# Performance work log

Hardware: AMD Instinct MI355X
Metric: run time of the kernel (lower is better)

The kernel has to match this reference:

```python
import jax, jax.numpy as jnp
import numpy as np

THRESH = 0.3
LENS = 0.4
DECAY = 0.2


@jax.custom_vjp
def act_fun(x):
    return (x > THRESH).astype(x.dtype)

def _act_fwd(x):
    return act_fun(x), x

def _act_bwd(x, g):
    return (g * (jnp.abs(x - THRESH) < LENS).astype(g.dtype),)

act_fun.defvjp(_act_fwd, _act_bwd)


def _conv(x, w):
    # 3x3, stride 1, padding 1, NCHW/OIHW (no bias)
    return jax.lax.conv_general_dilated(
        x, w, (1, 1), ((1, 1), (1, 1)),
        dimension_numbers=("NCHW", "OIHW", "NCHW"))


def _pool2(x):
    # avg_pool2d(k=2) applied per trailing hh-channel: x is (B,C,H,W,4)
    B, C, H, W, K = x.shape
    return x.reshape(B, C, H // 2, 2, W // 2, 2, K).mean(axis=(3, 5))


def _mem_update(x, mem, spike):
    m = mem * DECAY * (1.0 - spike) + x
    return m, act_fun(m)


def _lif_step(drives3, inner, mem, spike):
    # drives3: 3 conv drives (B,C,H,W); inner drives channel 3
    ms, ss = [], []
    for k in range(3):
        m, s = _mem_update(drives3[k], mem[..., k], spike[..., k])
        ms.append(m); ss.append(s)
    m, s = _mem_update(inner, mem[..., 3], spike[..., 3])
    ms.append(m); ss.append(s)
    return jnp.stack(ms, axis=-1), jnp.stack(ss, axis=-1)


def setup_inputs() -> dict:
    key = jax.random.key(0)
    ks = jax.random.split(key, 11)
    B, T = 256, 3
    sc = 0.1
    return {
        "x": jax.random.normal(ks[0], (B, 1, 36, 36), jnp.float32),
        "w1": jax.random.normal(ks[1], (3, 10, 1, 3, 3), jnp.float32) * sc,
        "b1": jax.random.normal(ks[2], (3, 10), jnp.float32) * sc,
        "w2": jax.random.normal(ks[3], (3, 10, 10, 3, 3), jnp.float32) * sc,
        "b2": jax.random.normal(ks[4], (3, 10), jnp.float32) * sc,
        "lif_w": jax.random.normal(ks[5], (1, 3), jnp.float32) * sc,
        "lif_b": jax.random.normal(ks[6], (1,), jnp.float32) * sc,
        "fc_w": jax.random.normal(ks[7], (50, 3240), jnp.float32) * 0.02,
        "fc_b": jax.random.normal(ks[8], (50,), jnp.float32) * sc,
        "task_w": jax.random.normal(ks[9], (T, 10, 50), jnp.float32) * sc,
        "task_b": jax.random.normal(ks[10], (T, 10), jnp.float32) * sc,
        "time_window": 10,
    }


def reference(x, w1, b1, w2, b2, lif_w, lif_b, fc_w, fc_b, task_w, task_b, time_window):
    B = x.shape[0]
    c1_mem = jnp.zeros((B, 10, 36, 36, 4), x.dtype)
    c1_spk = jnp.zeros_like(c1_mem)
    c2_mem = jnp.zeros((B, 10, 18, 18, 4), x.dtype)
    c2_spk = jnp.zeros_like(c2_mem)
    h1 = jnp.zeros((B, 3240), x.dtype)

    # layer-1 drives depend only on the (constant) input: compute once
    drives1 = [_conv(x, w1[k]) + b1[k][:, None, None] for k in range(3)]

    def step(carry, _):
        c1_mem, c1_spk, c2_mem, c2_spk, h1 = carry
        # layer 1 (is_spike_input=False)
        inner1 = jnp.einsum("bchwk,ok->bchwo", c1_mem[..., 0:3], lif_w)[..., 0] + lif_b[0]
        c1_mem_n, c1_spk_n = _lif_step(drives1, inner1, c1_mem, c1_spk)
        p1 = _pool2(c1_spk_n)  # (B,10,18,18,4)
        # layer 2 (is_spike_input=True): sum of conv over 4 slices = conv(sum)+4*bias
        s = p1.sum(axis=-1)
        drives2 = [_conv(s, w2[k]) + 4.0 * b2[k][:, None, None] for k in range(3)]
        inner2 = jnp.einsum("bchwk,ok->bchwo", c2_mem[..., 0:3], lif_w)[..., 0] + lif_b[0]
        c2_mem_n, c2_spk_n = _lif_step(drives2, inner2, c2_mem, c2_spk)
        p2 = _pool2(c2_spk_n)  # (B,10,9,9,4)
        h1 = h1 + p2.reshape(B, -1)
        return (c1_mem_n, c1_spk_n, c2_mem_n, c2_spk_n, h1), None

    carry, _ = jax.lax.scan(step, (c1_mem, c1_spk, c2_mem, c2_spk, h1), None, length=time_window)
    h1 = carry[4]
    outs = (h1 / time_window) @ fc_w.T + fc_b  # (B,50)
    out = jnp.einsum("bf,tof->bto", outs, task_w) + task_b[None]  # (B,T,10)
    return out
```

## Files before the change

### kernel.cpp

```cpp
#include <hip/hip_runtime.h>

#define TH  0.3f
#define DEC 0.2f

#define OFF_X    0
#define OFF_W1   1596
#define OFF_B1   1876
#define OFF_W2   1908
#define OFF_B2   4708
#define OFF_LIF  4740
#define OFF_S    4744
#define OFF_C1X  9944
#define OFF_C2   12800
#define SMEM_N   26570

__device__ __forceinline__ float spikef(float v) { return v > TH ? 1.f : 0.f; }

__device__ __forceinline__ float ag_w(float v) {
    float a;
    asm("v_accvgpr_write_b32 %0, %1" : "=a"(a) : "v"(v));
    return a;
}
__device__ __forceinline__ float ag_r(float a) {
    float v;
    asm("v_accvgpr_read_b32 %0, %1" : "=v"(v) : "a"(a));
    return v;
}

#define AG16_DECL(P) \
    float P##0=ag_w(0.f), P##1=ag_w(0.f), P##2=ag_w(0.f), P##3=ag_w(0.f),   \
          P##4=ag_w(0.f), P##5=ag_w(0.f), P##6=ag_w(0.f), P##7=ag_w(0.f),   \
          P##8=ag_w(0.f), P##9=ag_w(0.f), P##10=ag_w(0.f), P##11=ag_w(0.f), \
          P##12=ag_w(0.f), P##13=ag_w(0.f), P##14=ag_w(0.f), P##15=ag_w(0.f)

#define LIF4(M, D0, D1, D2)                                            \
    {                                                                  \
        float inner_ = fmaf((M).x, lw0, fmaf((M).y, lw1, fmaf((M).z, lw2, lb))); \
        (M).x = ((M).x > TH ? 0.f : (M).x * DEC) + (D0);               \
        (M).y = ((M).y > TH ? 0.f : (M).y * DEC) + (D1);               \
        (M).z = ((M).z > TH ? 0.f : (M).z * DEC) + (D2);               \
        (M).w = ((M).w > TH ? 0.f : (M).w * DEC) + inner_;             \
    }

#define CONV27(WB, ACC)                                                      \
    do {                                                                     \
        float4 w4_;                                                          \
        _Pragma("unroll")                                                    \
        for (int j_ = 0; j_ < 27; ++j_) {                                    \
            if ((j_ & 3) == 0)                                               \
                w4_ = *reinterpret_cast<const float4*>(&sm[(WB) + j_]);      \
            const float wv_ = ((j_ & 3) == 0) ? w4_.x :                      \
                              ((j_ & 3) == 1) ? w4_.y :                      \
                              ((j_ & 3) == 2) ? w4_.z : w4_.w;               \
            const int k_ = j_ / 9, r_ = (j_ - k_ * 9) / 3,                   \
                      c_ = j_ - k_ * 9 - r_ * 3;                             \
            ACC(k_, r_, c_, wv_);                                            \
        }                                                                    \
    } while (0)

#define ACC_L1(K, R, C, W)                                   \
    d[0][K] = fmaf(xv[R][C],         (W), d[0][K]);          \
    d[1][K] = fmaf(xv[R][C + 1],     (W), d[1][K]);          \
    d[2][K] = fmaf(xv[R + 1][C],     (W), d[2][K]);          \
    d[3][K] = fmaf(xv[R + 1][C + 1], (W), d[3][K]);

#define ACC_L2(K, R, C, W)                                   \
    acc[0][K] = fmaf(sv[R][C],         (W), acc[0][K]);      \
    acc[1][K] = fmaf(sv[R][C + 1],     (W), acc[1][K]);      \
    acc[2][K] = fmaf(sv[R + 1][C],     (W), acc[2][K]);      \
    acc[3][K] = fmaf(sv[R + 1][C + 1], (W), acc[3][K]);

__device__ __forceinline__ void conv1(const float* __restrict__ sm, int cell,
                                      float (&d)[4][3])
{
    int oc  = cell / 324;
    int rem = cell - oc * 324;
    int hh  = rem / 18;
    int ww  = rem - hh * 18;
    int y0 = 2 * hh, x0 = 2 * ww;

    float xv[4][4];
#pragma unroll
    for (int r = 0; r < 4; ++r) {
        float2 a = *reinterpret_cast<const float2*>(&sm[OFF_X + (y0 + r) * 42 + x0]);
        float2 b = *reinterpret_cast<const float2*>(&sm[OFF_X + (y0 + r) * 42 + x0 + 2]);
        xv[r][0] = a.x; xv[r][1] = a.y; xv[r][2] = b.x; xv[r][3] = b.y;
    }
    {
        float b0  = sm[OFF_B1 + oc];
        float b1v = sm[OFF_B1 + 10 + oc];
        float b2v = sm[OFF_B1 + 20 + oc];
#pragma unroll
        for (int p = 0; p < 4; ++p) { d[p][0] = b0; d[p][1] = b1v; d[p][2] = b2v; }
    }
    CONV27(OFF_W1 + oc * 28, ACC_L1);
}

__device__ __forceinline__ void conv2(const float* __restrict__ sm, int cell,
                                      float (&acc)[4][3])
{
    int oc  = cell / 81;
    int rem = cell - oc * 81;
    int hh  = rem / 9;
    int ww  = rem - hh * 9;
    int y0 = 2 * hh, x0 = 2 * ww;

    {
        float b20 = 4.f * sm[OFF_B2 + oc];
        float b21 = 4.f * sm[OFF_B2 + 10 + oc];
        float b22 = 4.f * sm[OFF_B2 + 20 + oc];
#pragma unroll
        for (int p = 0; p < 4; ++p) { acc[p][0] = b20; acc[p][1] = b21; acc[p][2] = b22; }
    }

    const int sb = OFF_S + y0 * 26 + x0;
    const int wb = OFF_W2 + (oc * 10) * 28;

    for (int ic = 0; ic < 10; ++ic) {
        float sv[4][4];
#pragma unroll
        for (int r = 0; r < 4; ++r) {
            float2 a = *reinterpret_cast<const float2*>(&sm[sb + ic * 520 + r * 26]);
            float2 b = *reinterpret_cast<const float2*>(&sm[sb + ic * 520 + r * 26 + 2]);
            sv[r][0] = a.x; sv[r][1] = a.y; sv[r][2] = b.x; sv[r][3] = b.y;
        }
        CONV27(wb + ic * 28, ACC_L2);
    }
}

#define L1_AG_CELL(P, CELL)                                                   \
    {                                                                         \
        const int cell_ = (CELL);                                             \
        float d[4][3];                                                        \
        conv1(sm, cell_, d);                                                  \
        float ssum = 0.f; float4 m;                                           \
        m = make_float4(ag_r(P##0), ag_r(P##1), ag_r(P##2), ag_r(P##3));      \
        LIF4(m, d[0][0], d[0][1], d[0][2]);                                   \
        ssum += spikef(m.x) + spikef(m.y) + spikef(m.z) + spikef(m.w);        \
        P##0=ag_w(m.x); P##1=ag_w(m.y); P##2=ag_w(m.z); P##3=ag_w(m.w);       \
        m = make_float4(ag_r(P##4), ag_r(P##5), ag_r(P##6), ag_r(P##7));      \
        LIF4(m, d[1][0], d[1][1], d[1][2]);                                   \
        ssum += spikef(m.x) + spikef(m.y) + spikef(m.z) + spikef(m.w);        \
        P##4=ag_w(m.x); P##5=ag_w(m.y); P##6=ag_w(m.z); P##7=ag_w(m.w);       \
        m = make_float4(ag_r(P##8), ag_r(P##9), ag_r(P##10), ag_r(P##11));    \
        LIF4(m, d[2][0], d[2][1], d[2][2]);                                   \
        ssum += spikef(m.x) + spikef(m.y) + spikef(m.z) + spikef(m.w);        \
        P##8=ag_w(m.x); P##9=ag_w(m.y); P##10=ag_w(m.z); P##11=ag_w(m.w);     \
        m = make_float4(ag_r(P##12), ag_r(P##13), ag_r(P##14), ag_r(P##15));  \
        LIF4(m, d[3][0], d[3][1], d[3][2]);                                   \
        ssum += spikef(m.x) + spikef(m.y) + spikef(m.z) + spikef(m.w);        \
        P##12=ag_w(m.x); P##13=ag_w(m.y); P##14=ag_w(m.z); P##15=ag_w(m.w);   \
        int oc_ = cell_ / 324, rem_ = cell_ - oc_ * 324;                      \
        int hh_ = rem_ / 18, ww_ = rem_ - hh_ * 18;                           \
        sm[OFF_S + oc_ * 520 + (hh_ + 1) * 26 + (ww_ + 1)] = ssum * 0.25f;    \
    }

__attribute__((amdgpu_waves_per_eu(4, 4)))
__global__ __launch_bounds__(1024)
void scnn_kernel(const float* __restrict__ x,
                 const float* __restrict__ w1, const float* __restrict__ b1,
                 const float* __restrict__ w2, const float* __restrict__ b2,
                 const float* __restrict__ lif_w, const float* __restrict__ lif_b,
                 const float* __restrict__ fc_w, const float* __restrict__ fc_b,
                 const float* __restrict__ task_w, const float* __restrict__ task_b,
                 const int* __restrict__ tw_ptr,
                 float* __restrict__ out)
{
    __shared__ float sm[SMEM_N];
    const int tid = threadIdx.x;
    const int b   = blockIdx.x;
    const int T   = tw_ptr[0];

    for (int i = tid; i < SMEM_N; i += 1024) sm[i] = 0.f;
    __syncthreads();

    for (int i = tid; i < 1296; i += 1024) {
        int h = i / 36, w = i - h * 36;
        sm[OFF_X + (h + 1) * 42 + (w + 1)] = x[b * 1296 + i];
    }
    if (tid < 270) {
        int k = tid / 90, r = tid - k * 90;
        int oc = r / 9, j = r - oc * 9;
        sm[OFF_W1 + oc * 28 + k * 9 + j] = w1[tid];
    }
    if (tid < 30)  sm[OFF_B1 + tid] = b1[tid];
    for (int i = tid; i < 2700; i += 1024) {
        int k = i / 900, r1 = i - k * 900;
        int oc = r1 / 90, r2 = r1 - oc * 90;
        int ic = r2 / 9,  j  = r2 - ic * 9;
        sm[OFF_W2 + (oc * 10 + ic) * 28 + k * 9 + j] = w2[i];
    }
    if (tid < 30)  sm[OFF_B2 + tid] = b2[tid];
    if (tid < 3)   sm[OFF_LIF + tid] = lif_w[tid];
    if (tid == 0)  sm[OFF_LIF + 3] = lif_b[0];
    __syncthreads();

    const float lw0 = sm[OFF_LIF + 0], lw1 = sm[OFF_LIF + 1],
                lw2 = sm[OFF_LIF + 2], lb  = sm[OFF_LIF + 3];

    AG16_DECL(aA);
    AG16_DECL(aB);
    AG16_DECL(aC);
    float hA0=0.f,hA1=0.f,hA2=0.f,hA3=0.f;

    for (int t = 0; t < T; ++t) {
        L1_AG_CELL(aA, tid);
        __builtin_amdgcn_sched_barrier(0);
        L1_AG_CELL(aB, tid + 1024);
        __builtin_amdgcn_sched_barrier(0);
        L1_AG_CELL(aC, tid + 2048);
        __builtin_amdgcn_sched_barrier(0);
        if (tid < 3240 - 3072) {
            const int cell = tid + 3072;
            float d[4][3];
            conv1(sm, cell, d);
            float* cp = &sm[OFF_C1X + tid * 17];
            float ssum = 0.f;
#pragma unroll
            for (int p = 0; p < 4; ++p) {
                float4 m = make_float4(cp[4*p], cp[4*p+1], cp[4*p+2], cp[4*p+3]);
                LIF4(m, d[p][0], d[p][1], d[p][2]);
                ssum += spikef(m.x) + spikef(m.y) + spikef(m.z) + spikef(m.w);
                cp[4*p] = m.x; cp[4*p+1] = m.y; cp[4*p+2] = m.z; cp[4*p+3] = m.w;
            }
            int oc_ = cell / 324, rem_ = cell - oc_ * 324;
            int hh_ = rem_ / 18, ww_ = rem_ - hh_ * 18;
            sm[OFF_S + oc_ * 520 + (hh_ + 1) * 26 + (ww_ + 1)] = ssum * 0.25f;
        }
        __syncthreads();

        if (tid < 810) {
            float acc[4][3];
            conv2(sm, tid, acc);
            float* cp = &sm[OFF_C2 + tid * 17];
#pragma unroll
            for (int p = 0; p < 4; ++p) {
                float4 m = make_float4(cp[4*p], cp[4*p+1], cp[4*p+2], cp[4*p+3]);
                LIF4(m, acc[p][0], acc[p][1], acc[p][2]);
                hA0 += spikef(m.x) * 0.25f; hA1 += spikef(m.y) * 0.25f;
                hA2 += spikef(m.z) * 0.25f; hA3 += spikef(m.w) * 0.25f;
                cp[4*p] = m.x; cp[4*p+1] = m.y; cp[4*p+2] = m.z; cp[4*p+3] = m.w;
            }
        }
        __syncthreads();
    }

    if (tid < 810)
        *reinterpret_cast<float4*>(&sm[OFF_S + tid * 4]) = make_float4(hA0, hA1, hA2, hA3);
    __syncthreads();

    float invT = 1.f / (float)T;
    int f = tid >> 4, g = tid & 15;
    if (f < 50) {
        const float* wrow = fc_w + f * 3240;
        float p0 = 0.f, p1 = 0.f;
        for (int j = g; j + 16 < 3240; j += 32) {
            p0 = fmaf(sm[OFF_S + j], wrow[j], p0);
            p1 = fmaf(sm[OFF_S + j + 16], wrow[j + 16], p1);
        }
        { int j = 3232 + g; if (j < 3240) p0 = fmaf(sm[OFF_S + j], wrow[j], p0); }
        float p = p0 + p1;
        p += __shfl_xor(p, 1);
        p += __shfl_xor(p, 2);
        p += __shfl_xor(p, 4);
        p += __shfl_xor(p, 8);
        if (g == 0) sm[OFF_X + f] = p * invT + fc_b[f];
    }
    __syncthreads();

    if (tid < 30) {
        float acc = task_b[tid];
        const float* twp = task_w + tid * 50;
        for (int j = 0; j < 50; ++j) acc = fmaf(sm[OFF_X + j], twp[j], acc);
        out[b * 30 + tid] = acc;
    }
}

extern "C" void kernel_launch(void* const* d_in, const int* in_sizes, int n_in,
                              void* d_out, int out_size, void* d_ws, size_t ws_size,
                              hipStream_t stream) {
    const float* x      = (const float*)d_in[0];
    const float* w1     = (const float*)d_in[1];
    const float* b1     = (const float*)d_in[2];
    const float* w2     = (const float*)d_in[3];
    const float* b2     = (const float*)d_in[4];
    const float* lif_w  = (const float*)d_in[5];
    const float* lif_b  = (const float*)d_in[6];
    const float* fc_w   = (const float*)d_in[7];
    const float* fc_b   = (const float*)d_in[8];
    const float* task_w = (const float*)d_in[9];
    const float* task_b = (const float*)d_in[10];
    const int*   tw     = (const int*)d_in[11];

    int B = in_sizes[0] / 1296;

    scnn_kernel<<<B, 1024, 0, stream>>>(x, w1, b1, w2, b2, lif_w, lif_b,
                                        fc_w, fc_b, task_w, task_b, tw,
                                        (float*)d_out);
}
```

Measured before the change: 204.8 us.

## Double-buffer layer-1 spike map to remove one barrier per time step

Adds a second pooled-spike buffer in shared memory and software-pipelines the time loop. Layer-2 conv for step t reads one buffer while layer-1 for step t+1 writes the other, so one __syncthreads per iteration is dropped. Threads 810 and up no longer idle at a barrier during the layer-2 phase, and layer-1 work can overlap with it. The cost is about 20KB more LDS, which could limit blocks per CU, and a peeled first layer-1 pass.

```diff
diff --git a/kernel.cpp b/kernel.cpp
--- a/kernel.cpp
+++ b/kernel.cpp
@@ -9,10 +9,11 @@
 #define OFF_W2   1908
 #define OFF_B2   4708
 #define OFF_LIF  4740
-#define OFF_S    4744
-#define OFF_C1X  9944
-#define OFF_C2   12800
-#define SMEM_N   26570
+#define OFF_SA   4744
+#define OFF_SB   9944
+#define OFF_C1X  15144
+#define OFF_C2   18000
+#define SMEM_N   31770
 
 __device__ __forceinline__ float spikef(float v) { return v > TH ? 1.f : 0.f; }
 
@@ -96,7 +97,7 @@
     CONV27(OFF_W1 + oc * 28, ACC_L1);
 }
 
-__device__ __forceinline__ void conv2(const float* __restrict__ sm, int cell,
+__device__ __forceinline__ void conv2(const float* __restrict__ sm, int sbase, int cell,
                                       float (&acc)[4][3])
 {
     int oc  = cell / 81;
@@ -113,7 +114,7 @@
         for (int p = 0; p < 4; ++p) { acc[p][0] = b20; acc[p][1] = b21; acc[p][2] = b22; }
     }
 
-    const int sb = OFF_S + y0 * 26 + x0;
+    const int sb = sbase + y0 * 26 + x0;
     const int wb = OFF_W2 + (oc * 10) * 28;
 
     for (int ic = 0; ic < 10; ++ic) {
@@ -128,7 +129,7 @@
     }
 }
 
-#define L1_AG_CELL(P, CELL)                                                   \
+#define L1_AG_CELL(P, CELL, SB_)                                              \
     {                                                                         \
         const int cell_ = (CELL);                                             \
         float d[4][3];                                                        \
@@ -152,8 +153,28 @@
         P##12=ag_w(m.x); P##13=ag_w(m.y); P##14=ag_w(m.z); P##15=ag_w(m.w);   \
         int oc_ = cell_ / 324, rem_ = cell_ - oc_ * 324;                      \
         int hh_ = rem_ / 18, ww_ = rem_ - hh_ * 18;                           \
-        sm[OFF_S + oc_ * 520 + (hh_ + 1) * 26 + (ww_ + 1)] = ssum * 0.25f;    \
-    }
+        sm[(SB_) + oc_ * 520 + (hh_ + 1) * 26 + (ww_ + 1)] = ssum * 0.25f;    \
+    }
+
+__device__ __forceinline__ void l1_overflow(float* __restrict__ sm, int tid, int sbase,
+                                            float lw0, float lw1, float lw2, float lb)
+{
+    const int cell = tid + 3072;
+    float d[4][3];
+    conv1(sm, cell, d);
+    float* cp = &sm[OFF_C1X + tid * 17];
+    float ssum = 0.f;
+#pragma unroll
+    for (int p = 0; p < 4; ++p) {
+        float4 m = make_float4(cp[4*p], cp[4*p+1], cp[4*p+2], cp[4*p+3]);
+        LIF4(m, d[p][0], d[p][1], d[p][2]);
+        ssum += spikef(m.x) + spikef(m.y) + spikef(m.z) + spikef(m.w);
+        cp[4*p] = m.x; cp[4*p+1] = m.y; cp[4*p+2] = m.z; cp[4*p+3] = m.w;
+    }
+    int oc_ = cell / 324, rem_ = cell - oc_ * 324;
+    int hh_ = rem_ / 18, ww_ = rem_ - hh_ * 18;
+    sm[sbase + oc_ * 520 + (hh_ + 1) * 26 + (ww_ + 1)] = ssum * 0.25f;
+}
 
 __attribute__((amdgpu_waves_per_eu(4, 4)))
 __global__ __launch_bounds__(1024)
@@ -203,35 +224,22 @@
     AG16_DECL(aC);
     float hA0=0.f,hA1=0.f,hA2=0.f,hA3=0.f;
 
+    L1_AG_CELL(aA, tid,        OFF_SA);
+    __builtin_amdgcn_sched_barrier(0);
+    L1_AG_CELL(aB, tid + 1024, OFF_SA);
+    __builtin_amdgcn_sched_barrier(0);
+    L1_AG_CELL(aC, tid + 2048, OFF_SA);
+    __builtin_amdgcn_sched_barrier(0);
+    if (tid < 3240 - 3072) l1_overflow(sm, tid, OFF_SA, lw0, lw1, lw2, lb);
+    __syncthreads();
+
     for (int t = 0; t < T; ++t) {
-        L1_AG_CELL(aA, tid);
-        __builtin_amdgcn_sched_barrier(0);
-        L1_AG_CELL(aB, tid + 1024);
-        __builtin_amdgcn_sched_barrier(0);
-        L1_AG_CELL(aC, tid + 2048);
-        __builtin_amdgcn_sched_barrier(0);
-        if (tid < 3240 - 3072) {
-            const int cell = tid + 3072;
-            float d[4][3];
-            conv1(sm, cell, d);
-            float* cp = &sm[OFF_C1X + tid * 17];
-            float ssum = 0.f;
-#pragma unroll
-            for (int p = 0; p < 4; ++p) {
-                float4 m = make_float4(cp[4*p], cp[4*p+1], cp[4*p+2], cp[4*p+3]);
-                LIF4(m, d[p][0], d[p][1], d[p][2]);
-                ssum += spikef(m.x) + spikef(m.y) + spikef(m.z) + spikef(m.w);
-                cp[4*p] = m.x; cp[4*p+1] = m.y; cp[4*p+2] = m.z; cp[4*p+3] = m.w;
-            }
-            int oc_ = cell / 324, rem_ = cell - oc_ * 324;
-            int hh_ = rem_ / 18, ww_ = rem_ - hh_ * 18;
-            sm[OFF_S + oc_ * 520 + (hh_ + 1) * 26 + (ww_ + 1)] = ssum * 0.25f;
-        }
-        __syncthreads();
+        const int scur = (t & 1) ? OFF_SB : OFF_SA;
+        const int snxt = (t & 1) ? OFF_SA : OFF_SB;
 
         if (tid < 810) {
             float acc[4][3];
-            conv2(sm, tid, acc);
+            conv2(sm, scur, tid, acc);
             float* cp = &sm[OFF_C2 + tid * 17];
 #pragma unroll
             for (int p = 0; p < 4; ++p) {
@@ -242,11 +250,22 @@
                 cp[4*p] = m.x; cp[4*p+1] = m.y; cp[4*p+2] = m.z; cp[4*p+3] = m.w;
             }
         }
+        __builtin_amdgcn_sched_barrier(0);
+
+        if (t + 1 < T) {
+            L1_AG_CELL(aA, tid,        snxt);
+            __builtin_amdgcn_sched_barrier(0);
+            L1_AG_CELL(aB, tid + 1024, snxt);
+            __builtin_amdgcn_sched_barrier(0);
+            L1_AG_CELL(aC, tid + 2048, snxt);
+            __builtin_amdgcn_sched_barrier(0);
+            if (tid < 3240 - 3072) l1_overflow(sm, tid, snxt, lw0, lw1, lw2, lb);
+        }
         __syncthreads();
     }
 
     if (tid < 810)
-        *reinterpret_cast<float4*>(&sm[OFF_S + tid * 4]) = make_float4(hA0, hA1, hA2, hA3);
+        *reinterpret_cast<float4*>(&sm[OFF_SA + tid * 4]) = make_float4(hA0, hA1, hA2, hA3);
     __syncthreads();
 
     float invT = 1.f / (float)T;
@@ -255,10 +274,10 @@
         const float* wrow = fc_w + f * 3240;
         float p0 = 0.f, p1 = 0.f;
         for (int j = g; j + 16 < 3240; j += 32) {
-            p0 = fmaf(sm[OFF_S + j], wrow[j], p0);
-            p1 = fmaf(sm[OFF_S + j + 16], wrow[j + 16], p1);
+            p0 = fmaf(sm[OFF_SA + j], wrow[j], p0);
+            p1 = fmaf(sm[OFF_SA + j + 16], wrow[j + 16], p1);
         }
-        { int j = 3232 + g; if (j < 3240) p0 = fmaf(sm[OFF_S + j], wrow[j], p0); }
+        { int j = 3232 + g; if (j < 3240) p0 = fmaf(sm[OFF_SA + j], wrow[j], p0); }
         float p = p0 + p1;
         p += __shfl_xor(p, 1);
         p += __shfl_xor(p, 2);
```

New measurement: 212.9 us. 1.04x slower.

## Use wave-uniform scalar weight loads for conv and remap layer-2 cells per wave

Applied to the files above, without the earlier changes.

Adds a small pre-kernel that writes the conv weights to workspace in a padded per-output-channel layout. When all lanes of a wave share an output channel, the main kernel reads those weights from global memory through uniform (scalar) loads instead of LDS. Layer-2 cells are reassigned so that each of the first 10 waves handles one output channel, which makes the weight index uniform across the wave. The remaining cells take the old LDS path, and the change adds an extra kernel launch and a divergence check in conv1.

```diff
diff --git a/kernel.cpp b/kernel.cpp
--- a/kernel.cpp
+++ b/kernel.cpp
@@ -58,6 +58,17 @@
         }                                                                    \
     } while (0)
 
+#define CONV27G(WP, ACC)                                                     \
+    do {                                                                     \
+        _Pragma("unroll")                                                    \
+        for (int j_ = 0; j_ < 27; ++j_) {                                    \
+            const float wv_ = (WP)[j_];                                      \
+            const int k_ = j_ / 9, r_ = (j_ - k_ * 9) / 3,                   \
+                      c_ = j_ - k_ * 9 - r_ * 3;                             \
+            ACC(k_, r_, c_, wv_);                                            \
+        }                                                                    \
+    } while (0)
+
 #define ACC_L1(K, R, C, W)                                   \
     d[0][K] = fmaf(xv[R][C],         (W), d[0][K]);          \
     d[1][K] = fmaf(xv[R][C + 1],     (W), d[1][K]);          \
@@ -70,8 +81,9 @@
     acc[2][K] = fmaf(sv[R + 1][C],     (W), acc[2][K]);      \
     acc[3][K] = fmaf(sv[R + 1][C + 1], (W), acc[3][K]);
 
-__device__ __forceinline__ void conv1(const float* __restrict__ sm, int cell,
-                                      float (&d)[4][3])
+__device__ __forceinline__ void conv1_core(const float* __restrict__ sm,
+                                           const float* __restrict__ w1g,
+                                           int cell, float (&d)[4][3])
 {
     int oc  = cell / 324;
     int rem = cell - oc * 324;
@@ -93,18 +105,20 @@
 #pragma unroll
         for (int p = 0; p < 4; ++p) { d[p][0] = b0; d[p][1] = b1v; d[p][2] = b2v; }
     }
-    CONV27(OFF_W1 + oc * 28, ACC_L1);
-}
-
-__device__ __forceinline__ void conv2(const float* __restrict__ sm, int cell,
-                                      float (&acc)[4][3])
-{
-    int oc  = cell / 81;
-    int rem = cell - oc * 81;
-    int hh  = rem / 9;
-    int ww  = rem - hh * 9;
-    int y0 = 2 * hh, x0 = 2 * ww;
-
+    int oc0 = __builtin_amdgcn_readfirstlane(oc);
+    if (__all(oc == oc0)) {
+        const float* wp = w1g + oc0 * 28;
+        CONV27G(wp, ACC_L1);
+    } else {
+        CONV27(OFF_W1 + oc * 28, ACC_L1);
+    }
+}
+
+__device__ __forceinline__ void conv2_g(const float* __restrict__ sm,
+                                        const float* __restrict__ wocg,
+                                        int oc, int hh, int ww,
+                                        float (&acc)[4][3])
+{
     {
         float b20 = 4.f * sm[OFF_B2 + oc];
         float b21 = 4.f * sm[OFF_B2 + 10 + oc];
@@ -112,10 +126,7 @@
 #pragma unroll
         for (int p = 0; p < 4; ++p) { acc[p][0] = b20; acc[p][1] = b21; acc[p][2] = b22; }
     }
-
-    const int sb = OFF_S + y0 * 26 + x0;
-    const int wb = OFF_W2 + (oc * 10) * 28;
-
+    const int sb = OFF_S + (2 * hh) * 26 + 2 * ww;
     for (int ic = 0; ic < 10; ++ic) {
         float sv[4][4];
 #pragma unroll
@@ -124,7 +135,49 @@
             float2 b = *reinterpret_cast<const float2*>(&sm[sb + ic * 520 + r * 26 + 2]);
             sv[r][0] = a.x; sv[r][1] = a.y; sv[r][2] = b.x; sv[r][3] = b.y;
         }
+        const float* wp = wocg + ic * 28;
+        CONV27G(wp, ACC_L2);
+    }
+}
+
+__device__ __forceinline__ void conv2_l(const float* __restrict__ sm,
+                                        int oc, int hh, int ww,
+                                        float (&acc)[4][3])
+{
+    {
+        float b20 = 4.f * sm[OFF_B2 + oc];
+        float b21 = 4.f * sm[OFF_B2 + 10 + oc];
+        float b22 = 4.f * sm[OFF_B2 + 20 + oc];
+#pragma unroll
+        for (int p = 0; p < 4; ++p) { acc[p][0] = b20; acc[p][1] = b21; acc[p][2] = b22; }
+    }
+    const int sb = OFF_S + (2 * hh) * 26 + 2 * ww;
+    const int wb = OFF_W2 + (oc * 10) * 28;
+    for (int ic = 0; ic < 10; ++ic) {
+        float sv[4][4];
+#pragma unroll
+        for (int r = 0; r < 4; ++r) {
+            float2 a = *reinterpret_cast<const float2*>(&sm[sb + ic * 520 + r * 26]);
+            float2 b = *reinterpret_cast<const float2*>(&sm[sb + ic * 520 + r * 26 + 2]);
+            sv[r][0] = a.x; sv[r][1] = a.y; sv[r][2] = b.x; sv[r][3] = b.y;
+        }
         CONV27(wb + ic * 28, ACC_L2);
+    }
+}
+
+__device__ __forceinline__ void l2_finish(float* __restrict__ sm, int cell,
+                                          float (&acc)[4][3],
+                                          float lw0, float lw1, float lw2, float lb,
+                                          float& h0, float& h1, float& h2, float& h3)
+{
+    float* cp = &sm[OFF_C2 + cell * 17];
+#pragma unroll
+    for (int p = 0; p < 4; ++p) {
+        float4 m = make_float4(cp[4*p], cp[4*p+1], cp[4*p+2], cp[4*p+3]);
+        LIF4(m, acc[p][0], acc[p][1], acc[p][2]);
+        h0 += spikef(m.x) * 0.25f; h1 += spikef(m.y) * 0.25f;
+        h2 += spikef(m.z) * 0.25f; h3 += spikef(m.w) * 0.25f;
+        cp[4*p] = m.x; cp[4*p+1] = m.y; cp[4*p+2] = m.z; cp[4*p+3] = m.w;
     }
 }
 
@@ -132,7 +185,7 @@
     {                                                                         \
         const int cell_ = (CELL);                                             \
         float d[4][3];                                                        \
-        conv1(sm, cell_, d);                                                  \
+        conv1_core(sm, w1g, cell_, d);                                        \
         float ssum = 0.f; float4 m;                                           \
         m = make_float4(ag_r(P##0), ag_r(P##1), ag_r(P##2), ag_r(P##3));      \
         LIF4(m, d[0][0], d[0][1], d[0][2]);                                   \
@@ -155,6 +208,24 @@
         sm[OFF_S + oc_ * 520 + (hh_ + 1) * 26 + (ww_ + 1)] = ssum * 0.25f;    \
     }
 
+__global__ __launch_bounds__(1024)
+void reorder_kernel(const float* __restrict__ w1, const float* __restrict__ w2,
+                    float* __restrict__ wsf)
+{
+    int tid = threadIdx.x;
+    if (tid < 270) {
+        int k = tid / 90, r = tid - k * 90;
+        int oc = r / 9, j = r - oc * 9;
+        wsf[oc * 28 + k * 9 + j] = w1[tid];
+    }
+    for (int i = tid; i < 2700; i += 1024) {
+        int k = i / 900, r1 = i - k * 900;
+        int oc = r1 / 90, r2 = r1 - oc * 90;
+        int ic = r2 / 9,  j  = r2 - ic * 9;
+        wsf[512 + (oc * 10 + ic) * 28 + k * 9 + j] = w2[i];
+    }
+}
+
 __attribute__((amdgpu_waves_per_eu(4, 4)))
 __global__ __launch_bounds__(1024)
 void scnn_kernel(const float* __restrict__ x,
@@ -164,12 +235,15 @@
                  const float* __restrict__ fc_w, const float* __restrict__ fc_b,
                  const float* __restrict__ task_w, const float* __restrict__ task_b,
                  const int* __restrict__ tw_ptr,
-                 float* __restrict__ out)
+                 float* __restrict__ out, const float* __restrict__ wsf)
 {
     __shared__ float sm[SMEM_N];
     const int tid = threadIdx.x;
     const int b   = blockIdx.x;
     const int T   = tw_ptr[0];
+
+    const float* w1g = wsf;
+    const float* w2g = wsf + 512;
 
     for (int i = tid; i < SMEM_N; i += 1024) sm[i] = 0.f;
     __syncthreads();
@@ -197,6 +271,23 @@
 
     const float lw0 = sm[OFF_LIF + 0], lw1 = sm[OFF_LIF + 1],
                 lw2 = sm[OFF_LIF + 2], lb  = sm[OFF_LIF + 3];
+
+    const int wv_id = __builtin_amdgcn_readfirstlane(tid >> 6);
+    const int lane  = tid & 63;
+    int l2cell = -1, l2oc = 0, l2hh = 0, l2ww = 0;
+    if (wv_id < 10) {
+        l2oc = wv_id;
+        l2cell = l2oc * 81 + lane;
+        l2hh = lane / 9; l2ww = lane - l2hh * 9;
+    } else if (wv_id < 13) {
+        int r = (wv_id - 10) * 64 + lane;
+        if (r < 170) {
+            l2oc = r / 17;
+            int j = 64 + (r - l2oc * 17);
+            l2cell = l2oc * 81 + j;
+            l2hh = j / 9; l2ww = j - l2hh * 9;
+        }
+    }
 
     AG16_DECL(aA);
     AG16_DECL(aB);
@@ -213,7 +304,7 @@
         if (tid < 3240 - 3072) {
             const int cell = tid + 3072;
             float d[4][3];
-            conv1(sm, cell, d);
+            conv1_core(sm, w1g, cell, d);
             float* cp = &sm[OFF_C1X + tid * 17];
             float ssum = 0.f;
 #pragma unroll
@@ -229,24 +320,20 @@
         }
         __syncthreads();
 
-        if (tid < 810) {
+        if (l2cell >= 0) {
             float acc[4][3];
-            conv2(sm, tid, acc);
-            float* cp = &sm[OFF_C2 + tid * 17];
-#pragma unroll
-            for (int p = 0; p < 4; ++p) {
-                float4 m = make_float4(cp[4*p], cp[4*p+1], cp[4*p+2], cp[4*p+3]);
-                LIF4(m, acc[p][0], acc[p][1], acc[p][2]);
-                hA0 += spikef(m.x) * 0.25f; hA1 += spikef(m.y) * 0.25f;
-                hA2 += spikef(m.z) * 0.25f; hA3 += spikef(m.w) * 0.25f;
-                cp[4*p] = m.x; cp[4*p+1] = m.y; cp[4*p+2] = m.z; cp[4*p+3] = m.w;
+            if (wv_id < 10) {
+                conv2_g(sm, w2g + l2oc * 280, l2oc, l2hh, l2ww, acc);
+            } else {
+                conv2_l(sm, l2oc, l2hh, l2ww, acc);
             }
+            l2_finish(sm, l2cell, acc, lw0, lw1, lw2, lb, hA0, hA1, hA2, hA3);
         }
         __syncthreads();
     }
 
-    if (tid < 810)
-        *reinterpret_cast<float4*>(&sm[OFF_S + tid * 4]) = make_float4(hA0, hA1, hA2, hA3);
+    if (l2cell >= 0)
+        *reinterpret_cast<float4*>(&sm[OFF_S + l2cell * 4]) = make_float4(hA0, hA1, hA2, hA3);
     __syncthreads();
 
     float invT = 1.f / (float)T;
@@ -294,7 +381,8 @@
 
     int B = in_sizes[0] / 1296;
 
+    reorder_kernel<<<1, 1024, 0, stream>>>(w1, w2, (float*)d_ws);
     scnn_kernel<<<B, 1024, 0, stream>>>(x, w1, b1, w2, b2, lif_w, lif_b,
                                         fc_w, fc_b, task_w, task_b, tw,
-                                        (float*)d_out);
-}
+                                        (float*)d_out, (const float*)d_ws);
+}
```

Measured after the change: 209.1 us. 1.02x slower.
